# Kernel tuning notes

Measured on AMD Instinct MI355X. Metric: run time of the kernel, lower is better.

The kernel has to match this reference:

```python
import jax, jax.numpy as jnp
import numpy as np
import math

B, S, H = 2, 2048, 2048
NH, HD = 16, 64  # head_dim = H // (2*NH)
LAMBDA_INIT = 0.5


def setup_inputs() -> dict:
    key = jax.random.key(0)
    ks = jax.random.split(key, 6)
    std = 1.0 / math.sqrt(H)
    hidden_states = jax.random.normal(ks[0], (B, S, H), dtype=jnp.float32)
    # Linear weights stored as [in, out] (x @ W)
    Wq = jax.random.normal(ks[1], (H, 2 * NH * HD), dtype=jnp.float32) * std
    Wk = jax.random.normal(ks[2], (H, 2 * NH * HD), dtype=jnp.float32) * std
    Wv = jax.random.normal(ks[3], (H, NH * HD), dtype=jnp.float32) * std
    Wo = jax.random.normal(ks[4], (NH * HD, H), dtype=jnp.float32) * (1.0 / math.sqrt(NH * HD))
    lambda_param = jnp.log(jnp.asarray(1.0 / math.tanh(LAMBDA_INIT), dtype=jnp.float32))
    # causal additive mask, (B, 1, S, S)
    causal = jnp.tril(jnp.ones((S, S), dtype=bool))
    attention_mask = jnp.where(causal, 0.0, jnp.finfo(jnp.float32).min)[None, None]
    attention_mask = jnp.broadcast_to(attention_mask, (B, 1, S, S))
    return {"hidden_states": hidden_states, "attention_mask": attention_mask,
            "Wq": Wq, "Wk": Wk, "Wv": Wv, "Wo": Wo, "lambda_param": lambda_param}


def reference(hidden_states, attention_mask, Wq, Wk, Wv, Wo, lambda_param):
    bsz, q_len, _ = hidden_states.shape
    scaling = HD ** -0.5

    q_all = (hidden_states @ Wq).reshape(bsz, q_len, 2 * NH, HD).transpose(0, 2, 1, 3)
    k_all = (hidden_states @ Wk).reshape(bsz, q_len, 2 * NH, HD).transpose(0, 2, 1, 3)
    v = (hidden_states @ Wv).reshape(bsz, q_len, NH, HD).transpose(0, 2, 1, 3)
    q1, q2 = q_all[:, :NH], q_all[:, NH:]
    k1, k2 = k_all[:, :NH], k_all[:, NH:]

    lam = jnp.tanh(jax.nn.softplus(lambda_param))
    scores1 = jnp.einsum('bhqd,bhkd->bhqk', q1, k1) * scaling
    scores2 = jnp.einsum('bhqd,bhkd->bhqk', q2, k2) * scaling
    attn_scores = scores1 - lam * scores2 + attention_mask
    attn_weights = jax.nn.softmax(attn_scores.astype(jnp.float32), axis=-1).astype(q1.dtype)

    attn_out = jnp.einsum('bhqk,bhkd->bhqd', attn_weights, v)
    attn_out = attn_out.transpose(0, 2, 1, 3).reshape(bsz, q_len, NH * HD)
    return attn_out @ Wo
```

## Files before the change

kernel.cpp:

```cpp
#include <hip/hip_runtime.h>
#include <hip/hip_bf16.h>

#define B_ 2
#define S_ 2048
#define H_ 2048
#define NH_ 16
#define HD_ 64
#define DQ_ 2048
#define DV_ 1024
#define QKS_ 4096

using bf16x8 = __attribute__((ext_vector_type(8))) __bf16;
using f32x4  = __attribute__((ext_vector_type(4))) float;

typedef __attribute__((address_space(1))) unsigned int u32g;
typedef __attribute__((address_space(3))) unsigned int u32l;

__device__ __forceinline__ void gload_lds16(const __bf16* g, __bf16* l) {
  __builtin_amdgcn_global_load_lds((u32g*)g, (u32l*)l, 16, 0, 0);
}

__device__ __forceinline__ int swz(int row, int colb, int strideB) {
  return row * strideB + (colb ^ (((row ^ (row >> 3)) & 7) << 4));
}
__device__ __forceinline__ int fxor(int row) { return (row ^ (row >> 3)) & 7; }


__global__ __launch_bounds__(256) void cast_hidden(const float* __restrict__ in,
                                                   __bf16* __restrict__ out, int n) {
  int i = (blockIdx.x * 256 + threadIdx.x) * 8;
  if (i >= n) return;
  float4 a = *reinterpret_cast<const float4*>(in + i);
  float4 b = *reinterpret_cast<const float4*>(in + i + 4);
  bf16x8 o;
  o[0] = (__bf16)a.x; o[1] = (__bf16)a.y; o[2] = (__bf16)a.z; o[3] = (__bf16)a.w;
  o[4] = (__bf16)b.x; o[5] = (__bf16)b.y; o[6] = (__bf16)b.z; o[7] = (__bf16)b.w;
  *reinterpret_cast<bf16x8*>(out + i) = o;
}

__global__ __launch_bounds__(256) void transpose_cast(const float* __restrict__ in,
                                                      __bf16* __restrict__ out, int R, int C) {
  __shared__ float tile[32][33];
  int tx = threadIdx.x & 31, ty = threadIdx.x >> 5;
  int c0 = blockIdx.x * 32, r0 = blockIdx.y * 32;
  for (int i = 0; i < 32; i += 8)
    tile[ty + i][tx] = in[(size_t)(r0 + ty + i) * C + c0 + tx];
  __syncthreads();
  for (int i = 0; i < 32; i += 8)
    out[(size_t)(c0 + ty + i) * R + r0 + tx] = (__bf16)tile[tx][ty + i];
}


template <typename OutT>
__global__ __launch_bounds__(256) void gemm_bt(const __bf16* __restrict__ A,
                                               const __bf16* __restrict__ Bt,
                                               OutT* __restrict__ C,
                                               int M, int N, int K) {
  __shared__ __bf16 As[2][128 * 32];
  __shared__ __bf16 Bs[2][128 * 32];
  const int nx = gridDim.x;
  int id = blockIdx.y * nx + blockIdx.x;
  const int cpx = (nx * gridDim.y) >> 3;
  id = (id & 7) * cpx + (id >> 3);
  const int bm = id / nx, bn = id % nx;

  const int tid = threadIdx.x;
  const int wid = tid >> 6, lane = tid & 63;
  const int wm = wid >> 1, wn = wid & 1;
  const int g = lane >> 4, c = lane & 15;

  f32x4 acc[4][4] = {};
  const __bf16* Abase = A + (size_t)(bm * 128) * K;
  const __bf16* Bbase = Bt + (size_t)(bn * 128) * K;
  const int srow = wid * 16 + (lane >> 2);
  const int scol = (lane & 3) * 8;
  const int nk = K >> 5;

  auto stage = [&](int p, int kt) {
    int k0 = kt * 32;
    gload_lds16(Abase + (size_t)srow * K + k0 + scol,        &As[p][(wid * 16) * 32]);
    gload_lds16(Abase + (size_t)(srow + 64) * K + k0 + scol, &As[p][(64 + wid * 16) * 32]);
    gload_lds16(Bbase + (size_t)srow * K + k0 + scol,        &Bs[p][(wid * 16) * 32]);
    gload_lds16(Bbase + (size_t)(srow + 64) * K + k0 + scol, &Bs[p][(64 + wid * 16) * 32]);
  };

  stage(0, 0);
  stage(1, 1);

  for (int kt = 0; kt < nk; ++kt) {
    const int p = kt & 1;
    if (kt + 1 < nk) {
      asm volatile("s_waitcnt vmcnt(4)" ::: "memory");
    } else {
      asm volatile("s_waitcnt vmcnt(0)" ::: "memory");
    }
    __builtin_amdgcn_s_barrier();
    __builtin_amdgcn_sched_barrier(0);

    bf16x8 af[4], bfv[4];
#pragma unroll
    for (int i = 0; i < 4; ++i)
      af[i] = *reinterpret_cast<const bf16x8*>(&As[p][(wm * 64 + i * 16 + c) * 32 + g * 8]);
#pragma unroll
    for (int i = 0; i < 4; ++i)
      bfv[i] = *reinterpret_cast<const bf16x8*>(&Bs[p][(wn * 64 + i * 16 + c) * 32 + g * 8]);
#pragma unroll
    for (int m = 0; m < 4; ++m)
#pragma unroll
      for (int n = 0; n < 4; ++n)
        acc[m][n] = __builtin_amdgcn_mfma_f32_16x16x32_bf16(af[m], bfv[n], acc[m][n], 0, 0, 0);

    __builtin_amdgcn_sched_barrier(0);
    __builtin_amdgcn_s_barrier();
    if (kt + 2 < nk) stage(p, kt + 2);
  }

#pragma unroll
  for (int m = 0; m < 4; ++m)
#pragma unroll
    for (int n = 0; n < 4; ++n)
#pragma unroll
      for (int r = 0; r < 4; ++r) {
        int row = bm * 128 + wm * 64 + m * 16 + g * 4 + r;
        int col = bn * 128 + wn * 64 + n * 16 + c;
        float v = acc[m][n][r];
        if constexpr (sizeof(OutT) == 2)
          C[(size_t)row * N + col] = (OutT)(__bf16)v;
        else
          C[(size_t)row * N + col] = v;
      }
}


__global__ __launch_bounds__(256, 2) void diffattn(const __bf16* __restrict__ QK,
                                                   const __bf16* __restrict__ V,
                                                   __bf16* __restrict__ OpA,
                                                   __bf16* __restrict__ OpB,
                                                   float* __restrict__ ml,
                                                   const float* __restrict__ lambda_param) {
  __shared__ __bf16 Ks[2][64 * 128];
  __shared__ __bf16 Vs[2][64 * 64];
  __shared__ __bf16 Ps[128 * 64];

  const int y = blockIdx.y;
  const int qt = ((y >> 4) & 1) ? blockIdx.x : (gridDim.x - 1 - blockIdx.x);
  const int bh = y >> 1;
  const int half = y & 1;
  const int b = bh >> 4, h = bh & 15;
  const int tid = threadIdx.x;
  const int w = tid >> 6, lane = tid & 63;
  const int g = lane >> 4, c = lane & 15;
  const float NEG_INF = -__builtin_inff();

  const float lam = tanhf(log1pf(__expf(lambda_param[0])));
  const float L2E = 1.4426950408889634f;
  const float sc1 = 0.125f * L2E;
  const float sc2 = -lam * 0.125f * L2E;

  bf16x8 qf[2][4];
#pragma unroll
  for (int fr = 0; fr < 2; ++fr) {
    int qrow = qt * 128 + w * 32 + fr * 16 + c;
    const __bf16* qbase = QK + (size_t)(b * S_ + qrow) * QKS_;
#pragma unroll
    for (int kk = 0; kk < 4; ++kk) {
      int d = kk * 32 + g * 8;
      const __bf16* src = (d < 64) ? (qbase + h * 64 + d)
                                   : (qbase + DV_ + h * 64 + (d - 64));
      float s = (d < 64) ? sc1 : sc2;
      bf16x8 raw = *reinterpret_cast<const bf16x8*>(src);
      bf16x8 ov;
#pragma unroll
      for (int i = 0; i < 8; ++i) ov[i] = (__bf16)((float)raw[i] * s);
      qf[fr][kk] = ov;
    }
  }

  f32x4 acc[2][4] = {};
  float mrow[2][4], lrow[2][4];
#pragma unroll
  for (int fr = 0; fr < 2; ++fr)
#pragma unroll
    for (int r = 0; r < 4; ++r) { mrow[fr][r] = -1e30f; lrow[fr][r] = 0.f; }

  const int kt0 = half ? (qt + 1) : 0;
  const int kt1 = half ? (2 * qt + 2) : (qt + 1);

  auto stageK = [&](int p, int kt) {
#pragma unroll
    for (int j = 0; j < 4; ++j) {
      int row = w * 16 + j * 4 + (lane >> 4);
      int gc = (lane & 15) ^ fxor(row);
      int s = kt * 64 + row;
      const __bf16* kbase = QK + (size_t)(b * S_ + s) * QKS_ + 2048;
      const __bf16* src = (gc < 8) ? (kbase + h * 64 + gc * 8)
                                   : (kbase + DV_ + h * 64 + (gc - 8) * 8);
      gload_lds16(src, &Ks[p][(w * 16 + j * 4) * 128]);
    }
  };
  auto loadV = [&](int kt, bf16x8* vv) {
#pragma unroll
    for (int j = 0; j < 2; ++j) {
      int flat = tid + j * 256;
      int kv = flat >> 3;
      int d = (flat & 7) * 8;
      vv[j] = *reinterpret_cast<const bf16x8*>(
          V + (size_t)(b * S_ + kt * 64 + kv) * DV_ + h * 64 + d);
    }
  };
  auto scatterV = [&](int p, const bf16x8* vv) {
    char* VsB = (char*)Vs[p];
#pragma unroll
    for (int j = 0; j < 2; ++j) {
      int flat = tid + j * 256;
      int kv = flat >> 3;
      int d = (flat & 7) * 8;
#pragma unroll
      for (int i = 0; i < 8; ++i)
        *reinterpret_cast<__bf16*>(VsB + swz(d + i, kv * 2, 128)) = vv[j][i];
    }
  };

  {
    stageK(0, kt0);
    bf16x8 vv[2];
    loadV(kt0, vv);
    scatterV(0, vv);
    __syncthreads();
  }

  for (int kt = kt0; kt < kt1; ++kt) {
    const int p = (kt - kt0) & 1;
    const bool pre = (kt + 1 < kt1);
    bf16x8 vv[2];
    if (pre) {
      stageK(p ^ 1, kt + 1);
      loadV(kt + 1, vv);
    }

    f32x4 sc[2][4] = {};
    char* KsB = (char*)Ks[p];
    __builtin_amdgcn_s_setprio(1);
#pragma unroll
    for (int f = 0; f < 4; ++f)
#pragma unroll
      for (int kk = 0; kk < 4; ++kk) {
        bf16x8 kf = *reinterpret_cast<const bf16x8*>(
            KsB + swz(f * 16 + c, (kk * 32 + g * 8) * 2, 256));
        sc[0][f] = __builtin_amdgcn_mfma_f32_16x16x32_bf16(qf[0][kk], kf, sc[0][f], 0, 0, 0);
        sc[1][f] = __builtin_amdgcn_mfma_f32_16x16x32_bf16(qf[1][kk], kf, sc[1][f], 0, 0, 0);
      }
    __builtin_amdgcn_s_setprio(0);

    const int dz = kt - 2 * qt;
#pragma unroll
    for (int fr = 0; fr < 2; ++fr) {
      const int wrow0 = w * 32 + fr * 16;
      float pmax[4] = {NEG_INF, NEG_INF, NEG_INF, NEG_INF};
      if (dz >= 0) {
#pragma unroll
        for (int f = 0; f < 4; ++f)
#pragma unroll
          for (int r = 0; r < 4; ++r) {
            float s = sc[fr][f][r];
            if (dz * 64 + f * 16 + c > wrow0 + g * 4 + r) s = NEG_INF;
            sc[fr][f][r] = s;
            pmax[r] = fmaxf(pmax[r], s);
          }
      } else {
#pragma unroll
        for (int f = 0; f < 4; ++f)
#pragma unroll
          for (int r = 0; r < 4; ++r)
            pmax[r] = fmaxf(pmax[r], sc[fr][f][r]);
      }
#pragma unroll
      for (int m = 1; m < 16; m <<= 1)
#pragma unroll
        for (int r = 0; r < 4; ++r)
          pmax[r] = fmaxf(pmax[r], __shfl_xor(pmax[r], m, 64));

      float dm = NEG_INF;
#pragma unroll
      for (int r = 0; r < 4; ++r) dm = fmaxf(dm, pmax[r] - mrow[fr][r]);
      if (!__all(dm <= 8.0f)) {
        float pscl[4];
#pragma unroll
        for (int r = 0; r < 4; ++r) {
          float mnew = fmaxf(mrow[fr][r], pmax[r]);
          pscl[r] = __builtin_amdgcn_exp2f(mrow[fr][r] - mnew);
          mrow[fr][r] = mnew;
        }
#pragma unroll
        for (int r = 0; r < 4; ++r) lrow[fr][r] *= pscl[r];
#pragma unroll
        for (int n = 0; n < 4; ++n)
#pragma unroll
          for (int r = 0; r < 4; ++r)
            acc[fr][n][r] *= pscl[r];
      }

      float rowsum[4] = {0.f, 0.f, 0.f, 0.f};
#pragma unroll
      for (int f = 0; f < 4; ++f)
#pragma unroll
        for (int r = 0; r < 4; ++r) {
          float pv = __builtin_amdgcn_exp2f(sc[fr][f][r] - mrow[fr][r]);
          sc[fr][f][r] = pv;
          rowsum[r] += pv;
        }
#pragma unroll
      for (int m = 1; m < 16; m <<= 1)
#pragma unroll
        for (int r = 0; r < 4; ++r)
          rowsum[r] += __shfl_xor(rowsum[r], m, 64);
#pragma unroll
      for (int r = 0; r < 4; ++r)
        lrow[fr][r] += rowsum[r];

      char* PsB = (char*)Ps;
#pragma unroll
      for (int f = 0; f < 4; ++f)
#pragma unroll
        for (int r = 0; r < 4; ++r)
          *reinterpret_cast<__bf16*>(
              PsB + swz(wrow0 + g * 4 + r, (f * 16 + c) * 2, 128)) = (__bf16)sc[fr][f][r];
    }

    {
      char* PsB = (char*)Ps;
      char* VsB = (char*)Vs[p];
      __builtin_amdgcn_s_setprio(1);
#pragma unroll
      for (int fr = 0; fr < 2; ++fr)
#pragma unroll
        for (int kc = 0; kc < 2; ++kc) {
          bf16x8 pf = *reinterpret_cast<const bf16x8*>(
              PsB + swz(w * 32 + fr * 16 + c, (kc * 32 + g * 8) * 2, 128));
#pragma unroll
          for (int n = 0; n < 4; ++n) {
            bf16x8 vf = *reinterpret_cast<const bf16x8*>(
                VsB + swz(n * 16 + c, (kc * 32 + g * 8) * 2, 128));
            acc[fr][n] = __builtin_amdgcn_mfma_f32_16x16x32_bf16(pf, vf, acc[fr][n], 0, 0, 0);
          }
        }
      __builtin_amdgcn_s_setprio(0);
    }

    if (pre) scatterV(p ^ 1, vv);
    __syncthreads();
  }

  __bf16* Op = half ? OpB : OpA;
#pragma unroll
  for (int fr = 0; fr < 2; ++fr)
#pragma unroll
    for (int n = 0; n < 4; ++n)
#pragma unroll
      for (int r = 0; r < 4; ++r) {
        int q = qt * 128 + w * 32 + fr * 16 + g * 4 + r;
        Op[(size_t)(b * S_ + q) * DV_ + h * 64 + n * 16 + c] = (__bf16)acc[fr][n][r];
      }
  if (c == 0) {
#pragma unroll
    for (int fr = 0; fr < 2; ++fr)
#pragma unroll
      for (int r = 0; r < 4; ++r) {
        int q = qt * 128 + w * 32 + fr * 16 + g * 4 + r;
        float2 v;
        v.x = mrow[fr][r];
        v.y = lrow[fr][r];
        *reinterpret_cast<float2*>(&ml[((size_t)(half * 32 + bh) * S_ + q) * 2]) = v;
      }
  }
}


__global__ __launch_bounds__(256) void merge_halves(const __bf16* __restrict__ OpA,
                                                    const __bf16* __restrict__ OpB,
                                                    const float* __restrict__ ml,
                                                    __bf16* __restrict__ AO) {
  int flat = blockIdx.x * 256 + threadIdx.x;
  int d0 = (flat & 7) * 8;
  int row = flat >> 3;
  int bh = row >> 11, q = row & 2047;
  int b = bh >> 4, h = bh & 15;
  size_t obase = (size_t)(b * S_ + q) * DV_ + h * 64 + d0;

  float2 a2 = *reinterpret_cast<const float2*>(&ml[((size_t)bh * S_ + q) * 2]);
  float2 b2 = *reinterpret_cast<const float2*>(&ml[((size_t)(32 + bh) * S_ + q) * 2]);
  float m = fmaxf(a2.x, b2.x);
  float wA = __builtin_amdgcn_exp2f(a2.x - m);
  float wB = __builtin_amdgcn_exp2f(b2.x - m);
  float inv = 1.0f / (a2.y * wA + b2.y * wB);
  wA *= inv; wB *= inv;

  bf16x8 oa = *reinterpret_cast<const bf16x8*>(OpA + obase);
  bf16x8 ob = *reinterpret_cast<const bf16x8*>(OpB + obase);
  bf16x8 o;
#pragma unroll
  for (int i = 0; i < 8; ++i)
    o[i] = (__bf16)((float)oa[i] * wA + (float)ob[i] * wB);
  *reinterpret_cast<bf16x8*>(AO + obase) = o;
}


extern "C" void kernel_launch(void* const* d_in, const int* in_sizes, int n_in,
                              void* d_out, int out_size, void* d_ws, size_t ws_size,
                              hipStream_t stream) {
  const float* hidden = (const float*)d_in[0];
  const float* Wq = (const float*)d_in[2];
  const float* Wk = (const float*)d_in[3];
  const float* Wv = (const float*)d_in[4];
  const float* Wo = (const float*)d_in[5];
  const float* lambda_param = (const float*)d_in[6];
  float* out = (float*)d_out;

  char* ws = (char*)d_ws;
  size_t off = 0;
  auto alloc = [&](size_t bytes) {
    void* p = ws + off;
    off += (bytes + 255) & ~(size_t)255;
    return p;
  };
  const int M = B_ * S_;
  __bf16* hidb = (__bf16*)alloc((size_t)M * H_ * 2);
  __bf16* TB   = (__bf16*)alloc((size_t)QKS_ * H_ * 2);
  __bf16* QKa  = (__bf16*)alloc((size_t)M * QKS_ * 2);
  __bf16* Va   = (__bf16*)((char*)TB + 4u * 1024 * 1024);
  float*  mlb  = (float*)((char*)TB + 12u * 1024 * 1024);
  __bf16* OpA  = hidb;
  __bf16* OpB  = hidb + (size_t)M * DV_;
  __bf16* AO   = hidb;
  (void)ws_size; (void)in_sizes; (void)n_in; (void)out_size;

  int nh = M * H_;
  cast_hidden<<<nh / (256 * 8), 256, 0, stream>>>(hidden, hidb, nh);

  transpose_cast<<<dim3(DQ_ / 32, H_ / 32), 256, 0, stream>>>(Wq, TB, H_, DQ_);
  transpose_cast<<<dim3(DQ_ / 32, H_ / 32), 256, 0, stream>>>(Wk, TB + (size_t)DQ_ * H_, H_, DQ_);
  gemm_bt<__bf16><<<dim3(QKS_ / 128, M / 128), 256, 0, stream>>>(hidb, TB, QKa, M, QKS_, H_);

  transpose_cast<<<dim3(DV_ / 32, H_ / 32), 256, 0, stream>>>(Wv, TB, H_, DV_);
  gemm_bt<__bf16><<<dim3(DV_ / 128, M / 128), 256, 0, stream>>>(hidb, TB, Va, M, DV_, H_);

  diffattn<<<dim3(S_ / 128, B_ * NH_ * 2), 256, 0, stream>>>(QKa, Va, OpA, OpB, mlb, lambda_param);
  merge_halves<<<(B_ * NH_ * S_ * HD_ / 8) / 256, 256, 0, stream>>>(OpA, OpB, mlb, AO);

  transpose_cast<<<dim3(H_ / 32, DV_ / 32), 256, 0, stream>>>(Wo, TB, DV_, H_);
  gemm_bt<float><<<dim3(H_ / 128, M / 128), 256, 0, stream>>>(AO, TB, out, M, H_, DV_);
}
```

Before: 284.4 us.

## Use 256x256-tile, 512-thread pipelined GEMM for the fused QK projection

Adds a new GEMM kernel with 256x256 output tiles, 8 waves and a double-buffered LDS pipeline. It interleaves global-to-LDS staging with quadrant-wise MFMA blocks, using barriers, priority hints and a tile-ID remap for L2 locality. It replaces the 128x128 GEMM for the large Q/K projection to get more data reuse per tile and to overlap loads with compute. In exchange it uses heavy LDS (128KB) and many registers, which limits occupancy, and only 128 blocks are launched on a device with many CUs.

```diff
diff --git a/kernel.cpp b/kernel.cpp
--- a/kernel.cpp
+++ b/kernel.cpp
@@ -24,6 +24,7 @@
   return row * strideB + (colb ^ (((row ^ (row >> 3)) & 7) << 4));
 }
 __device__ __forceinline__ int fxor(int row) { return (row ^ (row >> 3)) & 7; }
+__device__ __forceinline__ int fxor4(int row) { return (row ^ (row >> 2)) & 3; }
 
 
 __global__ __launch_bounds__(256) void cast_hidden(const float* __restrict__ in,
@@ -132,6 +133,152 @@
 }
 
 
+template <typename OutT>
+__global__ __launch_bounds__(512, 2) void gemm256(const __bf16* __restrict__ A,
+                                                  const __bf16* __restrict__ Bt,
+                                                  OutT* __restrict__ C,
+                                                  int M, int N, int K) {
+  __shared__ __bf16 As[2][256 * 64];
+  __shared__ __bf16 Bs[2][256 * 64];
+  const int nx = gridDim.x;
+  int id = blockIdx.y * nx + blockIdx.x;
+  const int cpx = (nx * gridDim.y) >> 3;
+  id = (id & 7) * cpx + (id >> 3);
+  const int bm = id / nx, bn = id % nx;
+
+  const int tid = threadIdx.x;
+  const int wid = tid >> 6, lane = tid & 63;
+  const int wm = wid >> 2, wn = wid & 3;
+  const int g = lane >> 4, c = lane & 15;
+
+  f32x4 acc[8][4] = {};
+  bf16x8 af[4][2];
+  bf16x8 bfv[4][2];
+  const __bf16* Abase = A + (size_t)(bm * 256) * K;
+  const __bf16* Bbase = Bt + (size_t)(bn * 256) * K;
+  const int niter = K >> 7;
+
+  auto stageA = [&](int p, int half, int kt) {
+#pragma unroll
+    for (int j = 0; j < 2; ++j) {
+      int row = half * 128 + j * 64 + wid * 8 + (lane >> 3);
+      int gc = (lane & 7) ^ (row & 7);
+      gload_lds16(Abase + (size_t)row * K + kt * 64 + gc * 8,
+                  &As[p][(half * 128 + j * 64 + wid * 8) * 64]);
+    }
+  };
+  auto stageB = [&](int p, int half, int kt) {
+#pragma unroll
+    for (int j = 0; j < 2; ++j) {
+      int row = half * 128 + j * 64 + wid * 8 + (lane >> 3);
+      int gc = (lane & 7) ^ (row & 7);
+      gload_lds16(Bbase + (size_t)row * K + kt * 64 + gc * 8,
+                  &Bs[p][(half * 128 + j * 64 + wid * 8) * 64]);
+    }
+  };
+  auto readA = [&](int p, int m, int kk) -> bf16x8 {
+    int row = wm * 128 + m * 16 + c;
+    int ch = (kk * 4 + g) ^ (row & 7);
+    return *reinterpret_cast<const bf16x8*>(&As[p][row * 64 + ch * 8]);
+  };
+  auto readB = [&](int p, int n, int kk) -> bf16x8 {
+    int row = wn * 64 + n * 16 + c;
+    int ch = (kk * 4 + g) ^ (row & 7);
+    return *reinterpret_cast<const bf16x8*>(&Bs[p][row * 64 + ch * 8]);
+  };
+  auto quad = [&](int mb, int nb) {
+    __builtin_amdgcn_s_setprio(1);
+#pragma unroll
+    for (int mi = 0; mi < 4; ++mi)
+#pragma unroll
+      for (int ni = 0; ni < 2; ++ni)
+#pragma unroll
+        for (int kk = 0; kk < 2; ++kk)
+          acc[mb + mi][nb + ni] = __builtin_amdgcn_mfma_f32_16x16x32_bf16(
+              af[mi][kk], bfv[nb + ni][kk], acc[mb + mi][nb + ni], 0, 0, 0);
+    __builtin_amdgcn_s_setprio(0);
+  };
+#define BAR1_LGKM()  __builtin_amdgcn_s_barrier(); \
+    asm volatile("s_waitcnt lgkmcnt(0)" ::: "memory"); \
+    __builtin_amdgcn_sched_barrier(0)
+#define BAR2()  __builtin_amdgcn_sched_barrier(0); __builtin_amdgcn_s_barrier()
+
+  stageA(0, 0, 0); stageA(0, 1, 0);
+  stageB(0, 0, 0); stageB(0, 1, 0);
+  stageB(1, 0, 1); stageB(1, 1, 1);
+  asm volatile("s_waitcnt vmcnt(0)" ::: "memory");
+  __builtin_amdgcn_s_barrier();
+
+  for (int i = 0; i < niter; ++i) {
+    const int t1 = 2 * i + 1;
+    const bool more = (i + 1 < niter);
+#pragma unroll
+    for (int mi = 0; mi < 4; ++mi) { af[mi][0] = readA(0, mi, 0); af[mi][1] = readA(0, mi, 1); }
+#pragma unroll
+    for (int ni = 0; ni < 2; ++ni) { bfv[ni][0] = readB(0, ni, 0); bfv[ni][1] = readB(0, ni, 1); }
+    stageA(1, 0, t1);
+    BAR1_LGKM(); quad(0, 0); BAR2();
+#pragma unroll
+    for (int ni = 2; ni < 4; ++ni) { bfv[ni][0] = readB(0, ni, 0); bfv[ni][1] = readB(0, ni, 1); }
+    stageA(1, 1, t1);
+    BAR1_LGKM(); quad(0, 2); BAR2();
+#pragma unroll
+    for (int mi = 0; mi < 4; ++mi) { af[mi][0] = readA(0, 4 + mi, 0); af[mi][1] = readA(0, 4 + mi, 1); }
+    if (more) stageB(0, 0, t1 + 1);
+    BAR1_LGKM(); quad(4, 0); BAR2();
+    if (more) {
+      stageB(0, 1, t1 + 1);
+      asm volatile("s_waitcnt vmcnt(4)" ::: "memory");
+    } else {
+      asm volatile("s_waitcnt vmcnt(0)" ::: "memory");
+    }
+    __builtin_amdgcn_s_barrier();
+    __builtin_amdgcn_sched_barrier(0);
+    quad(4, 2); BAR2();
+#pragma unroll
+    for (int mi = 0; mi < 4; ++mi) { af[mi][0] = readA(1, mi, 0); af[mi][1] = readA(1, mi, 1); }
+#pragma unroll
+    for (int ni = 0; ni < 2; ++ni) { bfv[ni][0] = readB(1, ni, 0); bfv[ni][1] = readB(1, ni, 1); }
+    if (more) stageA(0, 0, t1 + 1);
+    BAR1_LGKM(); quad(0, 0); BAR2();
+#pragma unroll
+    for (int ni = 2; ni < 4; ++ni) { bfv[ni][0] = readB(1, ni, 0); bfv[ni][1] = readB(1, ni, 1); }
+    if (more) stageA(0, 1, t1 + 1);
+    BAR1_LGKM(); quad(0, 2); BAR2();
+#pragma unroll
+    for (int mi = 0; mi < 4; ++mi) { af[mi][0] = readA(1, 4 + mi, 0); af[mi][1] = readA(1, 4 + mi, 1); }
+    if (more) stageB(1, 0, t1 + 2);
+    BAR1_LGKM(); quad(4, 0); BAR2();
+    if (more) {
+      stageB(1, 1, t1 + 2);
+      asm volatile("s_waitcnt vmcnt(4)" ::: "memory");
+    } else {
+      asm volatile("s_waitcnt vmcnt(0)" ::: "memory");
+    }
+    __builtin_amdgcn_s_barrier();
+    __builtin_amdgcn_sched_barrier(0);
+    quad(4, 2); BAR2();
+  }
+#undef BAR1_LGKM
+#undef BAR2
+
+#pragma unroll
+  for (int m = 0; m < 8; ++m)
+#pragma unroll
+    for (int n = 0; n < 4; ++n)
+#pragma unroll
+      for (int r = 0; r < 4; ++r) {
+        int row = bm * 256 + wm * 128 + m * 16 + g * 4 + r;
+        int col = bn * 256 + wn * 64 + n * 16 + c;
+        float v = acc[m][n][r];
+        if constexpr (sizeof(OutT) == 2)
+          C[(size_t)row * N + col] = (OutT)(__bf16)v;
+        else
+          C[(size_t)row * N + col] = v;
+      }
+}
+
+
 __global__ __launch_bounds__(256, 2) void diffattn(const __bf16* __restrict__ QK,
                                                    const __bf16* __restrict__ V,
                                                    __bf16* __restrict__ OpA,
@@ -439,7 +586,7 @@
 
   transpose_cast<<<dim3(DQ_ / 32, H_ / 32), 256, 0, stream>>>(Wq, TB, H_, DQ_);
   transpose_cast<<<dim3(DQ_ / 32, H_ / 32), 256, 0, stream>>>(Wk, TB + (size_t)DQ_ * H_, H_, DQ_);
-  gemm_bt<__bf16><<<dim3(QKS_ / 128, M / 128), 256, 0, stream>>>(hidb, TB, QKa, M, QKS_, H_);
+  gemm256<__bf16><<<dim3(QKS_ / 256, M / 256), 512, 0, stream>>>(hidb, TB, QKa, M, QKS_, H_);
 
   transpose_cast<<<dim3(DV_ / 32, H_ / 32), 256, 0, stream>>>(Wv, TB, H_, DV_);
   gemm_bt<__bf16><<<dim3(DV_ / 128, M / 128), 256, 0, stream>>>(hidb, TB, Va, M, DV_, H_);
```

After: 256.2 us. 9.9% less time.
